# Kernel tuning notes

Measured on AMD Instinct MI355X. Metric: run time of the kernel, lower is better.

The kernel has to match this reference:

```python
import jax, jax.numpy as jnp
import numpy as np

BN_EPS = 1e-5

def _conv(x, W, b, stride, pad):
    # x: [B,C,H,W], W: [O,I,kh,kw]
    y = jax.lax.conv_general_dilated(
        x, W, window_strides=(stride, stride),
        padding=[(pad, pad), (pad, pad)],
        dimension_numbers=('NCHW', 'OIHW', 'NCHW'))
    return y + b[None, :, None, None]

def _bn(x, gamma, beta, mean, var):
    inv = gamma * jax.lax.rsqrt(var + BN_EPS)
    return x * inv[None, :, None, None] + (beta - mean * inv)[None, :, None, None]

def _haar_cD(x):
    # pywt.dwt2(x, 'haar') diagonal detail over last two axes (even H,W):
    # cD[i,j] = (x[2i,2j] - x[2i,2j+1] - x[2i+1,2j] + x[2i+1,2j+1]) / 2
    a = x[..., 0::2, 0::2]
    b = x[..., 0::2, 1::2]
    c = x[..., 1::2, 0::2]
    d = x[..., 1::2, 1::2]
    return (a - b - c + d) * 0.5

def setup_inputs() -> dict:
    key = jax.random.key(0)
    ks = jax.random.split(key, 20)
    B = 8192
    f32 = jnp.float32
    inp = {
        'x':   jax.random.normal(ks[0], (B, 3, 32, 32), dtype=f32),
        # conv1: 3 -> 32, k5 s2 p2
        'w1':  jax.random.normal(ks[1], (32, 3, 5, 5), dtype=f32) * 0.05,
        'b1':  jnp.zeros((32,), f32),
        'g1':  jnp.ones((32,), f32),
        'be1': jnp.zeros((32,), f32),
        'm1':  jax.random.normal(ks[2], (32,), dtype=f32) * 0.1,
        'v1':  jax.random.uniform(ks[3], (32,), dtype=f32, minval=0.5, maxval=1.5),
        # conv2: 32 -> 64, k3 s2 p1
        'w2':  jax.random.normal(ks[4], (64, 32, 3, 3), dtype=f32) * 0.05,
        'b2':  jnp.zeros((64,), f32),
        'g2':  jnp.ones((64,), f32),
        'be2': jnp.zeros((64,), f32),
        'm2':  jax.random.normal(ks[5], (64,), dtype=f32) * 0.1,
        'v2':  jax.random.uniform(ks[6], (64,), dtype=f32, minval=0.5, maxval=1.5),
        # attention conv: 64 -> 1, k1
        'wa':  jax.random.normal(ks[7], (1, 64, 1, 1), dtype=f32) * 0.1,
        'ba':  jnp.zeros((1,), f32),
        # decoder linears (torch Linear layout: [out, in])
        'wd1': jax.random.normal(ks[8], (512, 64 * 8 * 8), dtype=f32) * 0.02,
        'bd1': jnp.zeros((512,), f32),
        'wd2': jax.random.normal(ks[9], (128, 512), dtype=f32) * 0.04,
        'bd2': jnp.zeros((128,), f32),
    }
    return inp

def reference(x, w1, b1, g1, be1, m1, v1, w2, b2, g2, be2, m2, v2,
              wa, ba, wd1, bd1, wd2, bd2):
    # wavelet_conv stem
    h = jax.nn.relu(_bn(_conv(x, w1, b1, 2, 2), g1, be1, m1, v1))   # [B,32,16,16]
    feat = jax.nn.relu(_bn(_conv(h, w2, b2, 2, 1), g2, be2, m2, v2))  # [B,64,8,8]
    # Haar DWT diagonal-detail gate (detached in the original)
    cD = jax.lax.stop_gradient(_haar_cD(feat))                        # [B,64,4,4]
    cD_up = jnp.repeat(jnp.repeat(cD, 2, axis=-2), 2, axis=-1)        # [B,64,8,8]
    feat = feat * cD_up
    # attention gate
    attn = jax.nn.sigmoid(_conv(feat, wa, ba, 1, 0))                  # [B,1,8,8]
    feat = feat * attn
    # decode
    f = feat.reshape(feat.shape[0], -1)                               # [B,4096]
    h1 = jax.nn.relu(f @ wd1.T + bd1)                                  # [B,512]
    return jax.nn.sigmoid(h1 @ wd2.T + bd2)                            # [B,128]
```

## Files before the change

### kernel.cpp

```cpp
#include <hip/hip_runtime.h>
#include <hip/hip_bf16.h>

typedef __bf16 bf16x8 __attribute__((ext_vector_type(8)));
typedef __bf16 bf16x4 __attribute__((ext_vector_type(4)));
typedef float f32x4 __attribute__((ext_vector_type(4)));

#define BN_EPS 1e-5f

__device__ __forceinline__ void gl_lds16(const __bf16* g, __bf16* l) {
    __builtin_amdgcn_global_load_lds(
        (const __attribute__((address_space(1))) unsigned int*)g,
        (__attribute__((address_space(3))) unsigned int*)l,
        16, 0, 0);
}

__global__ __launch_bounds__(256) void wd1p_kernel(const float* __restrict__ wd1, __bf16* __restrict__ o) {
    __shared__ float t2[64][65];
    const int n = blockIdx.x;
    const int tid = threadIdx.x;
    const float* src = wd1 + (size_t)n * 4096;
    #pragma unroll
    for (int r = 0; r < 16; ++r) {
        int j = r * 256 + tid;
        t2[j & 63][j >> 6] = src[j];
    }
    __syncthreads();
    __bf16* dst = o + (size_t)n * 4096;
    #pragma unroll
    for (int r = 0; r < 16; ++r) {
        int t = r * 256 + tid;
        dst[t] = (__bf16)t2[t >> 6][t & 63];
    }
}

__global__ void prep_kernel(const float* __restrict__ wd2, const float* __restrict__ w1,
                            const float* __restrict__ w2,
                            __bf16* __restrict__ wd2o, __bf16* __restrict__ w1o,
                            __bf16* __restrict__ w2o) {
    int i = blockIdx.x * 256 + threadIdx.x;
    if (i < 65536) { wd2o[i] = (__bf16)wd2[i]; return; }
    i -= 65536;
    if (i < 4096) {
        int oc = i >> 7, rem = i & 127;
        int ot = rem >> 3, j = rem & 7;
        float v = 0.f;
        if (ot < 15 && j < 5) {
            int ic = ot / 5, ky = ot % 5;
            v = w1[((oc * 3 + ic) * 5 + ky) * 5 + j];
        }
        w1o[i] = (__bf16)v;
        return;
    }
    i -= 4096;
    if (i < 18432) {
        int oc = i / 288, rem = i % 288;
        int tap = rem / 32, ic = rem % 32;
        w2o[i] = (__bf16)w2[(oc * 32 + ic) * 9 + tap];
    }
}

__global__ __launch_bounds__(512, 2) void conv_fused_kernel(
    const float* __restrict__ x,
    const __bf16* __restrict__ w1r, const float* __restrict__ b1,
    const float* __restrict__ g1, const float* __restrict__ be1,
    const float* __restrict__ m1, const float* __restrict__ v1,
    const __bf16* __restrict__ w2r, const float* __restrict__ b2,
    const float* __restrict__ g2, const float* __restrict__ be2,
    const float* __restrict__ m2, const float* __restrict__ v2,
    const float* __restrict__ wa, const float* __restrict__ ba,
    __bf16* __restrict__ f)
{
    __shared__ __align__(16) __bf16 xsb2[2][3 * 36 * 40];
    __shared__ __align__(16) char  ubuf2[2][23552];

    const int tid  = threadIdx.x;
    const int half = tid >> 8;
    const int t    = tid & 255;
    __bf16* xsb  = xsb2[half];
    char*   ubuf = ubuf2[half];
    __bf16* hsf  = (__bf16*)ubuf;
    float*  feat = (float*)ubuf;
    float*  cds  = (float*)(ubuf + 17408);
    float*  atn  = (float*)(ubuf + 22528);

    const int b    = blockIdx.x * 2 + half;
    const int lane = t & 63;
    const int wave = t >> 6;
    const int lo   = lane >> 4;
    const int ln   = lane & 15;

    {
        bf16x8 z = {};
        for (int i = t; i < 540; i += 256) *(bf16x8*)&xsb[i * 8] = z;
        if (t < 132) {
            int pi = t >> 2, ch = t & 3;
            int pix = (pi < 17) ? pi : (pi - 16) * 17;
            *(bf16x8*)&hsf[pix * 40 + ch * 8] = z;
        }
    }
    __syncthreads();

    {
        const float4* xb = (const float4*)(x + (size_t)b * 3072);
        #pragma unroll
        for (int r = 0; r < 3; ++r) {
            int c = r * 256 + t;
            int plane = c >> 8, rem = c & 255;
            int row = rem >> 3, c4 = rem & 7;
            float4 v = xb[c];
            bf16x4 h;
            h[0] = (__bf16)v.x; h[1] = (__bf16)v.y; h[2] = (__bf16)v.z; h[3] = (__bf16)v.w;
            *(bf16x4*)&xsb[plane * 1440 + (row + 2) * 40 + 4 + c4 * 4] = h;
        }
    }

    bf16x8 bw1[2][4];
    #pragma unroll
    for (int nt = 0; nt < 2; ++nt)
        #pragma unroll
        for (int s = 0; s < 4; ++s)
            bw1[nt][s] = *(const bf16x8*)(w1r + (nt * 16 + ln) * 128 + (s * 4 + lo) * 8);
    __syncthreads();

    f32x4 c1[4][2] = {};
    const unsigned int* xw = (const unsigned int*)xsb;
    #pragma unroll
    for (int s = 0; s < 4; ++s) {
        const int o  = s * 4 + lo;
        const int ic = (o * 205) >> 10;
        const int ky = o - ic * 5;
        const bool dummy = (o == 15);
        const int icc = dummy ? 2 : ic;
        #pragma unroll
        for (int mt = 0; mt < 4; ++mt) {
            const int oy  = wave * 4 + mt;
            const int row = dummy ? 35 : (2 * oy + ky);
            const int dw  = icc * 720 + row * 20 + ln + 1;
            union { unsigned int u[4]; bf16x8 v; } fa;
            fa.u[0] = xw[dw]; fa.u[1] = xw[dw + 1]; fa.u[2] = xw[dw + 2]; fa.u[3] = 0;
            #pragma unroll
            for (int nt = 0; nt < 2; ++nt)
                c1[mt][nt] = __builtin_amdgcn_mfma_f32_16x16x32_bf16(fa.v, bw1[nt][s], c1[mt][nt], 0, 0, 0);
        }
    }

    #pragma unroll
    for (int nt = 0; nt < 2; ++nt) {
        const int oc  = nt * 16 + ln;
        const float inv = g1[oc] * rsqrtf(v1[oc] + BN_EPS);
        const float bb  = be1[oc] + (b1[oc] - m1[oc]) * inv;
        #pragma unroll
        for (int mt = 0; mt < 4; ++mt) {
            const int hy = wave * 4 + mt + 1;
            #pragma unroll
            for (int r = 0; r < 4; ++r) {
                const int hx = lo * 4 + r + 1;
                hsf[(hy * 17 + hx) * 40 + oc] = (__bf16)fmaxf(c1[mt][nt][r] * inv + bb, 0.f);
            }
        }
    }

    const int wm = wave >> 1, wn = wave & 1;
    bf16x8 bw2[2][9];
    #pragma unroll
    for (int nt = 0; nt < 2; ++nt) {
        const __bf16* wp = w2r + (wn * 32 + nt * 16 + ln) * 288 + lo * 8;
        #pragma unroll
        for (int ks = 0; ks < 9; ++ks)
            bw2[nt][ks] = *(const bf16x8*)(wp + ks * 32);
    }
    __syncthreads();

    f32x4 c2[2][2] = {};
    {
        int pixbase[2];
        #pragma unroll
        for (int mt = 0; mt < 2; ++mt) {
            int p = wm * 32 + mt * 16 + ln;
            int qy = p >> 3, qx = p & 7;
            pixbase[mt] = (2 * qy * 17 + 2 * qx) * 40 + lo * 8;
        }
        #pragma unroll
        for (int ks = 0; ks < 9; ++ks) {
            const int ty = ks / 3, tx = ks % 3;
            bf16x8 af[2];
            #pragma unroll
            for (int mt = 0; mt < 2; ++mt)
                af[mt] = *(const bf16x8*)&hsf[pixbase[mt] + (ty * 17 + tx) * 40];
            #pragma unroll
            for (int mt = 0; mt < 2; ++mt)
                #pragma unroll
                for (int nt = 0; nt < 2; ++nt)
                    c2[mt][nt] = __builtin_amdgcn_mfma_f32_16x16x32_bf16(af[mt], bw2[nt][ks], c2[mt][nt], 0, 0, 0);
        }
    }
    __syncthreads();

    #pragma unroll
    for (int nt = 0; nt < 2; ++nt) {
        const int oc  = wn * 32 + nt * 16 + ln;
        const float inv = g2[oc] * rsqrtf(v2[oc] + BN_EPS);
        const float bb  = be2[oc] + (b2[oc] - m2[oc]) * inv;
        #pragma unroll
        for (int mt = 0; mt < 2; ++mt) {
            const int p0 = wm * 32 + mt * 16 + lo * 4;
            f32x4 o;
            #pragma unroll
            for (int r = 0; r < 4; ++r)
                o[r] = fmaxf(c2[mt][nt][r] * inv + bb, 0.f);
            *(f32x4*)&feat[oc * 68 + p0] = o;
        }
    }
    __syncthreads();

    {
        const int c = t >> 2, y = t & 3;
        const float* fr = feat + c * 68 + 16 * y;
        f32x4 t0 = *(const f32x4*)(fr);
        f32x4 t2v = *(const f32x4*)(fr + 4);
        f32x4 t1 = *(const f32x4*)(fr + 8);
        f32x4 t3 = *(const f32x4*)(fr + 12);
        f32x4 o;
        o[0] = 0.5f * (t0[0] - t0[1] - t1[0] + t1[1]);
        o[1] = 0.5f * (t0[2] - t0[3] - t1[2] + t1[3]);
        o[2] = 0.5f * (t2v[0] - t2v[1] - t3[0] + t3[1]);
        o[3] = 0.5f * (t2v[2] - t2v[3] - t3[2] + t3[3]);
        *(f32x4*)&cds[c * 20 + y * 4] = o;
    }
    __syncthreads();

    const int q  = t & 63;
    const int g  = wave;
    const int qy2 = q >> 3, qx2 = q & 7;
    const int qq = (qy2 >> 1) * 4 + (qx2 >> 1);
    float a2[16];
    float part = 0.f;
    #pragma unroll
    for (int j = 0; j < 16; ++j) {
        int oc = g * 16 + j;
        float v = feat[oc * 68 + q] * cds[oc * 20 + qq];
        a2[j] = v;
        part += v * wa[oc];
    }
    atn[g * 64 + q] = part;
    __syncthreads();
    float s2  = atn[q] + atn[64 + q] + atn[128 + q] + atn[192 + q] + ba[0];
    float sig = 1.f / (1.f + __expf(-s2));

    bf16x8 fo0, fo1;
    #pragma unroll
    for (int j = 0; j < 8; ++j) {
        fo0[j] = (__bf16)(a2[j] * sig);
        fo1[j] = (__bf16)(a2[j + 8] * sig);
    }
    __bf16* fb = f + (size_t)b * 4096 + q * 64 + g * 16;
    *(bf16x8*)fb = fo0;
    *(bf16x8*)(fb + 8) = fo1;
}

__global__ __launch_bounds__(256, 4) void gemm1_split_kernel(
    const __bf16* __restrict__ A, const __bf16* __restrict__ B,
    float* __restrict__ P)
{
    const int K = 4096, NOUT = 512, KH = 2048;
    __shared__ __align__(16) __bf16 As[64][64];
    __shared__ __align__(16) __bf16 Bs[128][64];
    const int tid  = threadIdx.x;
    const int lane = tid & 63;
    const int wave = tid >> 6;
    const int lo = lane >> 4, ln = lane & 15;
    const int bid = blockIdx.x;
    const int swz = (bid & 7) * 128 + (bid >> 3);
    const int n0  = (swz & 3) * 128;
    const int zz  = (swz >> 2) & 1;
    const int m0  = (swz >> 3) * 64;
    const int ks0 = zz * KH;
    const int sw = ln & 7;
    f32x4 acc[4][2] = {};
    for (int k0 = ks0; k0 < ks0 + KH; k0 += 64) {
        #pragma unroll
        for (int r = 0; r < 2; ++r) {
            int i = r * 256 + tid;
            int row = i >> 3, cs = i & 7;
            gl_lds16(A + (size_t)(m0 + row) * K + k0 + (cs ^ (row & 7)) * 8, &As[0][0] + i * 8);
        }
        #pragma unroll
        for (int r = 0; r < 4; ++r) {
            int i = r * 256 + tid;
            int row = i >> 3, cs = i & 7;
            gl_lds16(B + (size_t)(n0 + row) * K + k0 + (cs ^ (row & 7)) * 8, &Bs[0][0] + i * 8);
        }
        __syncthreads();
        #pragma unroll
        for (int s = 0; s < 2; ++s) {
            const int c = s * 4 + lo;
            const int slot = (c ^ sw) * 8;
            bf16x8 af[4], bfr[2];
            #pragma unroll
            for (int mt = 0; mt < 4; ++mt)
                af[mt] = *(const bf16x8*)(&As[mt * 16 + ln][slot]);
            #pragma unroll
            for (int nt = 0; nt < 2; ++nt)
                bfr[nt] = *(const bf16x8*)(&Bs[wave * 32 + nt * 16 + ln][slot]);
            #pragma unroll
            for (int mt = 0; mt < 4; ++mt)
                #pragma unroll
                for (int nt = 0; nt < 2; ++nt)
                    acc[mt][nt] = __builtin_amdgcn_mfma_f32_16x16x32_bf16(af[mt], bfr[nt], acc[mt][nt], 0, 0, 0);
        }
        __syncthreads();
    }
    float* Pp = P + (size_t)zz * 8192 * 512;
    #pragma unroll
    for (int mt = 0; mt < 4; ++mt)
        #pragma unroll
        for (int nt = 0; nt < 2; ++nt)
            #pragma unroll
            for (int r = 0; r < 4; ++r) {
                int m = m0 + mt * 16 + lo * 4 + r;
                int n = n0 + wave * 32 + nt * 16 + ln;
                Pp[(size_t)m * NOUT + n] = acc[mt][nt][r];
            }
}

__global__ __launch_bounds__(256) void gemm1_kernel(
    const __bf16* __restrict__ A, const __bf16* __restrict__ B,
    const float* __restrict__ bias, __bf16* __restrict__ C)
{
    const int K = 4096, NOUT = 512;
    __shared__ __align__(16) __bf16 As[64][64];
    __shared__ __align__(16) __bf16 Bs[128][64];
    const int tid  = threadIdx.x;
    const int lane = tid & 63;
    const int wave = tid >> 6;
    const int lo = lane >> 4, ln = lane & 15;
    const int bid = blockIdx.x;
    const int swz = (bid & 7) * 64 + (bid >> 3);
    const int n0  = (swz & 3) * 128;
    const int m0  = (swz >> 2) * 64;
    const int sw = ln & 7;
    f32x4 acc[4][2] = {};
    for (int k0 = 0; k0 < K; k0 += 64) {
        #pragma unroll
        for (int r = 0; r < 2; ++r) {
            int i = r * 256 + tid;
            int row = i >> 3, cs = i & 7;
            gl_lds16(A + (size_t)(m0 + row) * K + k0 + (cs ^ (row & 7)) * 8, &As[0][0] + i * 8);
        }
        #pragma unroll
        for (int r = 0; r < 4; ++r) {
            int i = r * 256 + tid;
            int row = i >> 3, cs = i & 7;
            gl_lds16(B + (size_t)(n0 + row) * K + k0 + (cs ^ (row & 7)) * 8, &Bs[0][0] + i * 8);
        }
        __syncthreads();
        #pragma unroll
        for (int s = 0; s < 2; ++s) {
            const int c = s * 4 + lo;
            const int slot = (c ^ sw) * 8;
            bf16x8 af[4], bfr[2];
            #pragma unroll
            for (int mt = 0; mt < 4; ++mt)
                af[mt] = *(const bf16x8*)(&As[mt * 16 + ln][slot]);
            #pragma unroll
            for (int nt = 0; nt < 2; ++nt)
                bfr[nt] = *(const bf16x8*)(&Bs[wave * 32 + nt * 16 + ln][slot]);
            #pragma unroll
            for (int mt = 0; mt < 4; ++mt)
                #pragma unroll
                for (int nt = 0; nt < 2; ++nt)
                    acc[mt][nt] = __builtin_amdgcn_mfma_f32_16x16x32_bf16(af[mt], bfr[nt], acc[mt][nt], 0, 0, 0);
        }
        __syncthreads();
    }
    #pragma unroll
    for (int mt = 0; mt < 4; ++mt)
        #pragma unroll
        for (int nt = 0; nt < 2; ++nt)
            #pragma unroll
            for (int r = 0; r < 4; ++r) {
                int m = m0 + mt * 16 + lo * 4 + r;
                int n = n0 + wave * 32 + nt * 16 + ln;
                float v = acc[mt][nt][r] + bias[n];
                C[(size_t)m * NOUT + n] = (__bf16)fmaxf(v, 0.f);
            }
}

__global__ __launch_bounds__(256, 4) void gemm2_kernel(
    const __bf16* __restrict__ A, const float* __restrict__ P,
    const float* __restrict__ bd1, const __bf16* __restrict__ B,
    const float* __restrict__ bias, float* __restrict__ Out, int fused)
{
    const int K = 512, NOUT = 128;
    __shared__ __align__(16) __bf16 As[32][64];
    __shared__ __align__(16) __bf16 Bs[128][64];
    const int tid  = threadIdx.x;
    const int lane = tid & 63;
    const int wave = tid >> 6;
    const int lo = lane >> 4, ln = lane & 15;
    const int m0 = blockIdx.x * 32;
    const int sw = ln & 7;
    const size_t HALF = (size_t)8192 * 512;
    f32x4 acc[2][2] = {};
    for (int k0 = 0; k0 < K; k0 += 64) {
        {
            int i = tid;
            int row = i >> 3, cs = i & 7;
            int k = k0 + (cs ^ (row & 7)) * 8;
            if (fused) {
                const float* p0 = P + (size_t)(m0 + row) * K + k;
                f32x4 a0 = *(const f32x4*)(p0);
                f32x4 a1 = *(const f32x4*)(p0 + 4);
                f32x4 c0 = *(const f32x4*)(p0 + HALF);
                f32x4 c1 = *(const f32x4*)(p0 + HALF + 4);
                f32x4 b0 = *(const f32x4*)(bd1 + k);
                f32x4 b1v = *(const f32x4*)(bd1 + k + 4);
                bf16x8 o;
                #pragma unroll
                for (int j = 0; j < 4; ++j) {
                    o[j]     = (__bf16)fmaxf(a0[j] + c0[j] + b0[j], 0.f);
                    o[j + 4] = (__bf16)fmaxf(a1[j] + c1[j] + b1v[j], 0.f);
                }
                *(bf16x8*)(&As[0][0] + i * 8) = o;
            } else {
                gl_lds16(A + (size_t)(m0 + row) * K + k, &As[0][0] + i * 8);
            }
        }
        #pragma unroll
        for (int r = 0; r < 4; ++r) {
            int i = r * 256 + tid;
            int row = i >> 3, cs = i & 7;
            gl_lds16(B + (size_t)row * K + k0 + (cs ^ (row & 7)) * 8, &Bs[0][0] + i * 8);
        }
        __syncthreads();
        #pragma unroll
        for (int s = 0; s < 2; ++s) {
            const int c = s * 4 + lo;
            const int slot = (c ^ sw) * 8;
            bf16x8 af[2], bfr[2];
            #pragma unroll
            for (int mt = 0; mt < 2; ++mt)
                af[mt] = *(const bf16x8*)(&As[mt * 16 + ln][slot]);
            #pragma unroll
            for (int nt = 0; nt < 2; ++nt)
                bfr[nt] = *(const bf16x8*)(&Bs[wave * 32 + nt * 16 + ln][slot]);
            #pragma unroll
            for (int mt = 0; mt < 2; ++mt)
                #pragma unroll
                for (int nt = 0; nt < 2; ++nt)
                    acc[mt][nt] = __builtin_amdgcn_mfma_f32_16x16x32_bf16(af[mt], bfr[nt], acc[mt][nt], 0, 0, 0);
        }
        __syncthreads();
    }
    #pragma unroll
    for (int mt = 0; mt < 2; ++mt)
        #pragma unroll
        for (int nt = 0; nt < 2; ++nt)
            #pragma unroll
            for (int r = 0; r < 4; ++r) {
                int m = m0 + mt * 16 + lo * 4 + r;
                int n = wave * 32 + nt * 16 + ln;
                float v = acc[mt][nt][r] + bias[n];
                Out[(size_t)m * NOUT + n] = 1.f / (1.f + __expf(-v));
            }
}

extern "C" void kernel_launch(void* const* d_in, const int* in_sizes, int n_in,
                              void* d_out, int out_size, void* d_ws, size_t ws_size,
                              hipStream_t stream)
{
    const float* x   = (const float*)d_in[0];
    const float* w1  = (const float*)d_in[1];
    const float* b1  = (const float*)d_in[2];
    const float* g1  = (const float*)d_in[3];
    const float* be1 = (const float*)d_in[4];
    const float* m1  = (const float*)d_in[5];
    const float* v1  = (const float*)d_in[6];
    const float* w2  = (const float*)d_in[7];
    const float* b2  = (const float*)d_in[8];
    const float* g2  = (const float*)d_in[9];
    const float* be2 = (const float*)d_in[10];
    const float* m2  = (const float*)d_in[11];
    const float* v2  = (const float*)d_in[12];
    const float* wa  = (const float*)d_in[13];
    const float* ba  = (const float*)d_in[14];
    const float* wd1 = (const float*)d_in[15];
    const float* bd1 = (const float*)d_in[16];
    const float* wd2 = (const float*)d_in[17];
    const float* bd2 = (const float*)d_in[18];

    char* ws = (char*)d_ws;
    const size_t SZ_F  = 67108864;
    const size_t SZ_P  = 33554432;
    const size_t SZ_H1 = 8388608;
    const bool use_split = ws_size >= (SZ_F + SZ_P + SZ_H1 + 4194304 + 131072 + 65536 + 8192);

    __bf16* f_bf = (__bf16*)ws;
    float*  P;
    __bf16* h1_bf;
    char* tail;
    if (use_split) {
        P      = (float*)(ws + SZ_F);
        h1_bf  = (__bf16*)(ws + SZ_F + SZ_P);
        tail   = ws + SZ_F + SZ_P + SZ_H1;
    } else {
        P      = nullptr;
        h1_bf  = (__bf16*)(ws + SZ_F);
        tail   = ws + SZ_F + SZ_H1;
    }
    __bf16* wd1_bf = (__bf16*)tail;
    __bf16* wd2_bf = (__bf16*)(tail + 4194304);
    __bf16* w2r_bf = (__bf16*)(tail + 4194304 + 131072);
    __bf16* w1r_bf = (__bf16*)(tail + 4194304 + 131072 + 65536);

    prep_kernel<<<344, 256, 0, stream>>>(wd2, w1, w2, wd2_bf, w1r_bf, w2r_bf);
    wd1p_kernel<<<512, 256, 0, stream>>>(wd1, wd1_bf);

    conv_fused_kernel<<<4096, 512, 0, stream>>>(x, w1r_bf, b1, g1, be1, m1, v1,
                                                w2r_bf, b2, g2, be2, m2, v2, wa, ba, f_bf);

    if (use_split) {
        gemm1_split_kernel<<<1024, 256, 0, stream>>>(f_bf, wd1_bf, P);
        gemm2_kernel<<<256, 256, 0, stream>>>(nullptr, P, bd1, wd2_bf, bd2, (float*)d_out, 1);
    } else {
        gemm1_kernel<<<512, 256, 0, stream>>>(f_bf, wd1_bf, bd1, h1_bf);
        gemm2_kernel<<<256, 256, 0, stream>>>(h1_bf, nullptr, bd1, wd2_bf, bd2, (float*)d_out, 0);
    }
}
```

Before: 311.2 us.

## Split conv blocks to one image each and double-buffer split GEMM1 LDS tiles

The fused conv kernel now launches one 256-thread block per image instead of packing two images into a 512-thread block, with launch bounds set for 5 blocks per CU. This gives the scheduler finer-grained blocks and makes each block independent of the other image's barriers. The split-K GEMM1 kernel double-buffers its A/B LDS tiles so the next K-slice's global-to-LDS loads are issued before the MFMAs on the current slice run. In exchange it doubles LDS per block and drops the occupancy hint from 4 to 3.

```diff
diff --git a/kernel.cpp b/kernel.cpp
--- a/kernel.cpp
+++ b/kernel.cpp
@@ -59,7 +59,7 @@
     }
 }
 
-__global__ __launch_bounds__(512, 2) void conv_fused_kernel(
+__global__ __launch_bounds__(256, 5) void conv_fused_kernel(
     const float* __restrict__ x,
     const __bf16* __restrict__ w1r, const float* __restrict__ b1,
     const float* __restrict__ g1, const float* __restrict__ be1,
@@ -70,30 +70,25 @@
     const float* __restrict__ wa, const float* __restrict__ ba,
     __bf16* __restrict__ f)
 {
-    __shared__ __align__(16) __bf16 xsb2[2][3 * 36 * 40];
-    __shared__ __align__(16) char  ubuf2[2][23552];
-
-    const int tid  = threadIdx.x;
-    const int half = tid >> 8;
-    const int t    = tid & 255;
-    __bf16* xsb  = xsb2[half];
-    char*   ubuf = ubuf2[half];
+    __shared__ __align__(16) __bf16 xsb[3 * 36 * 40];
+    __shared__ __align__(16) char  ubuf[23552];
     __bf16* hsf  = (__bf16*)ubuf;
     float*  feat = (float*)ubuf;
     float*  cds  = (float*)(ubuf + 17408);
     float*  atn  = (float*)(ubuf + 22528);
 
-    const int b    = blockIdx.x * 2 + half;
-    const int lane = t & 63;
-    const int wave = t >> 6;
+    const int b    = blockIdx.x;
+    const int tid  = threadIdx.x;
+    const int lane = tid & 63;
+    const int wave = tid >> 6;
     const int lo   = lane >> 4;
     const int ln   = lane & 15;
 
     {
         bf16x8 z = {};
-        for (int i = t; i < 540; i += 256) *(bf16x8*)&xsb[i * 8] = z;
-        if (t < 132) {
-            int pi = t >> 2, ch = t & 3;
+        for (int i = tid; i < 540; i += 256) *(bf16x8*)&xsb[i * 8] = z;
+        if (tid < 132) {
+            int pi = tid >> 2, ch = tid & 3;
             int pix = (pi < 17) ? pi : (pi - 16) * 17;
             *(bf16x8*)&hsf[pix * 40 + ch * 8] = z;
         }
@@ -104,7 +99,7 @@
         const float4* xb = (const float4*)(x + (size_t)b * 3072);
         #pragma unroll
         for (int r = 0; r < 3; ++r) {
-            int c = r * 256 + t;
+            int c = r * 256 + tid;
             int plane = c >> 8, rem = c & 255;
             int row = rem >> 3, c4 = rem & 7;
             float4 v = xb[c];
@@ -214,7 +209,7 @@
     __syncthreads();
 
     {
-        const int c = t >> 2, y = t & 3;
+        const int c = tid >> 2, y = tid & 3;
         const float* fr = feat + c * 68 + 16 * y;
         f32x4 t0 = *(const f32x4*)(fr);
         f32x4 t2v = *(const f32x4*)(fr + 4);
@@ -229,7 +224,7 @@
     }
     __syncthreads();
 
-    const int q  = t & 63;
+    const int q  = tid & 63;
     const int g  = wave;
     const int qy2 = q >> 3, qx2 = q & 7;
     const int qq = (qy2 >> 1) * 4 + (qx2 >> 1);
@@ -258,13 +253,13 @@
     *(bf16x8*)(fb + 8) = fo1;
 }
 
-__global__ __launch_bounds__(256, 4) void gemm1_split_kernel(
+__global__ __launch_bounds__(256, 3) void gemm1_split_kernel(
     const __bf16* __restrict__ A, const __bf16* __restrict__ B,
     float* __restrict__ P)
 {
     const int K = 4096, NOUT = 512, KH = 2048;
-    __shared__ __align__(16) __bf16 As[64][64];
-    __shared__ __align__(16) __bf16 Bs[128][64];
+    __shared__ __align__(16) __bf16 As[2][64][64];
+    __shared__ __align__(16) __bf16 Bs[2][128][64];
     const int tid  = threadIdx.x;
     const int lane = tid & 63;
     const int wave = tid >> 6;
@@ -276,21 +271,48 @@
     const int m0  = (swz >> 3) * 64;
     const int ks0 = zz * KH;
     const int sw = ln & 7;
+
+    const int arow = tid >> 3, acs = tid & 7;
+    const int aks  = (acs ^ (arow & 7)) * 8;
+    const int brow = tid >> 3, bcs = tid & 7;
+
     f32x4 acc[4][2] = {};
-    for (int k0 = ks0; k0 < ks0 + KH; k0 += 64) {
+
+    {
+        const int k0 = ks0;
         #pragma unroll
         for (int r = 0; r < 2; ++r) {
             int i = r * 256 + tid;
             int row = i >> 3, cs = i & 7;
-            gl_lds16(A + (size_t)(m0 + row) * K + k0 + (cs ^ (row & 7)) * 8, &As[0][0] + i * 8);
+            gl_lds16(A + (size_t)(m0 + row) * K + k0 + (cs ^ (row & 7)) * 8, &As[0][0][0] + i * 8);
         }
         #pragma unroll
         for (int r = 0; r < 4; ++r) {
             int i = r * 256 + tid;
             int row = i >> 3, cs = i & 7;
-            gl_lds16(B + (size_t)(n0 + row) * K + k0 + (cs ^ (row & 7)) * 8, &Bs[0][0] + i * 8);
-        }
-        __syncthreads();
+            gl_lds16(B + (size_t)(n0 + row) * K + k0 + (cs ^ (row & 7)) * 8, &Bs[0][0][0] + i * 8);
+        }
+    }
+    __syncthreads();
+
+    int cur = 0;
+    for (int k0 = ks0; k0 < ks0 + KH; k0 += 64) {
+        const int nxt = cur ^ 1;
+        if (k0 + 64 < ks0 + KH) {
+            const int k1 = k0 + 64;
+            #pragma unroll
+            for (int r = 0; r < 2; ++r) {
+                int i = r * 256 + tid;
+                int row = i >> 3, cs = i & 7;
+                gl_lds16(A + (size_t)(m0 + row) * K + k1 + (cs ^ (row & 7)) * 8, &As[nxt][0][0] + i * 8);
+            }
+            #pragma unroll
+            for (int r = 0; r < 4; ++r) {
+                int i = r * 256 + tid;
+                int row = i >> 3, cs = i & 7;
+                gl_lds16(B + (size_t)(n0 + row) * K + k1 + (cs ^ (row & 7)) * 8, &Bs[nxt][0][0] + i * 8);
+            }
+        }
         #pragma unroll
         for (int s = 0; s < 2; ++s) {
             const int c = s * 4 + lo;
@@ -298,10 +320,10 @@
             bf16x8 af[4], bfr[2];
             #pragma unroll
             for (int mt = 0; mt < 4; ++mt)
-                af[mt] = *(const bf16x8*)(&As[mt * 16 + ln][slot]);
+                af[mt] = *(const bf16x8*)(&As[cur][mt * 16 + ln][slot]);
             #pragma unroll
             for (int nt = 0; nt < 2; ++nt)
-                bfr[nt] = *(const bf16x8*)(&Bs[wave * 32 + nt * 16 + ln][slot]);
+                bfr[nt] = *(const bf16x8*)(&Bs[cur][wave * 32 + nt * 16 + ln][slot]);
             #pragma unroll
             for (int mt = 0; mt < 4; ++mt)
                 #pragma unroll
@@ -309,7 +331,9 @@
                     acc[mt][nt] = __builtin_amdgcn_mfma_f32_16x16x32_bf16(af[mt], bfr[nt], acc[mt][nt], 0, 0, 0);
         }
         __syncthreads();
-    }
+        cur = nxt;
+    }
+
     float* Pp = P + (size_t)zz * 8192 * 512;
     #pragma unroll
     for (int mt = 0; mt < 4; ++mt)
@@ -516,7 +540,7 @@
     prep_kernel<<<344, 256, 0, stream>>>(wd2, w1, w2, wd2_bf, w1r_bf, w2r_bf);
     wd1p_kernel<<<512, 256, 0, stream>>>(wd1, wd1_bf);
 
-    conv_fused_kernel<<<4096, 512, 0, stream>>>(x, w1r_bf, b1, g1, be1, m1, v1,
+    conv_fused_kernel<<<8192, 256, 0, stream>>>(x, w1r_bf, b1, g1, be1, m1, v1,
                                                 w2r_bf, b2, g2, be2, m2, v2, wa, ba, f_bf);
 
     if (use_split) {
```

After: 318.0 us. 2.2% more time.

## Split conv kernel to one sample per block and merge prep launches

Applied to the files above, without the earlier changes.

Conv kernel now processes one sample per 256-thread block rather than two samples per 512-thread block, with launch bounds requesting 5 blocks per CU, so finer-grained blocks can improve occupancy and scheduling. The two weight-prep kernels are merged into a single launch that dispatches by block index to remove one launch. The stricter occupancy hint may force register spilling, and each block still carries its own LDS buffers.

```diff
diff --git a/kernel.cpp b/kernel.cpp
--- a/kernel.cpp
+++ b/kernel.cpp
@@ -14,30 +14,33 @@
         16, 0, 0);
 }
 
-__global__ __launch_bounds__(256) void wd1p_kernel(const float* __restrict__ wd1, __bf16* __restrict__ o) {
+__global__ __launch_bounds__(256) void prep_all_kernel(
+    const float* __restrict__ wd1, __bf16* __restrict__ wd1o,
+    const float* __restrict__ wd2, const float* __restrict__ w1,
+    const float* __restrict__ w2,
+    __bf16* __restrict__ wd2o, __bf16* __restrict__ w1o,
+    __bf16* __restrict__ w2o)
+{
     __shared__ float t2[64][65];
-    const int n = blockIdx.x;
     const int tid = threadIdx.x;
-    const float* src = wd1 + (size_t)n * 4096;
-    #pragma unroll
-    for (int r = 0; r < 16; ++r) {
-        int j = r * 256 + tid;
-        t2[j & 63][j >> 6] = src[j];
-    }
-    __syncthreads();
-    __bf16* dst = o + (size_t)n * 4096;
-    #pragma unroll
-    for (int r = 0; r < 16; ++r) {
-        int t = r * 256 + tid;
-        dst[t] = (__bf16)t2[t >> 6][t & 63];
-    }
-}
-
-__global__ void prep_kernel(const float* __restrict__ wd2, const float* __restrict__ w1,
-                            const float* __restrict__ w2,
-                            __bf16* __restrict__ wd2o, __bf16* __restrict__ w1o,
-                            __bf16* __restrict__ w2o) {
-    int i = blockIdx.x * 256 + threadIdx.x;
+    if (blockIdx.x < 512) {
+        const int n = blockIdx.x;
+        const float* src = wd1 + (size_t)n * 4096;
+        #pragma unroll
+        for (int r = 0; r < 16; ++r) {
+            int j = r * 256 + tid;
+            t2[j & 63][j >> 6] = src[j];
+        }
+        __syncthreads();
+        __bf16* dst = wd1o + (size_t)n * 4096;
+        #pragma unroll
+        for (int r = 0; r < 16; ++r) {
+            int t = r * 256 + tid;
+            dst[t] = (__bf16)t2[t >> 6][t & 63];
+        }
+        return;
+    }
+    int i = (blockIdx.x - 512) * 256 + tid;
     if (i < 65536) { wd2o[i] = (__bf16)wd2[i]; return; }
     i -= 65536;
     if (i < 4096) {
@@ -59,7 +62,7 @@
     }
 }
 
-__global__ __launch_bounds__(512, 2) void conv_fused_kernel(
+__global__ __launch_bounds__(256, 5) void conv_fused_kernel(
     const float* __restrict__ x,
     const __bf16* __restrict__ w1r, const float* __restrict__ b1,
     const float* __restrict__ g1, const float* __restrict__ be1,
@@ -70,30 +73,25 @@
     const float* __restrict__ wa, const float* __restrict__ ba,
     __bf16* __restrict__ f)
 {
-    __shared__ __align__(16) __bf16 xsb2[2][3 * 36 * 40];
-    __shared__ __align__(16) char  ubuf2[2][23552];
-
-    const int tid  = threadIdx.x;
-    const int half = tid >> 8;
-    const int t    = tid & 255;
-    __bf16* xsb  = xsb2[half];
-    char*   ubuf = ubuf2[half];
+    __shared__ __align__(16) __bf16 xsb[3 * 36 * 40];
+    __shared__ __align__(16) char  ubuf[23552];
     __bf16* hsf  = (__bf16*)ubuf;
     float*  feat = (float*)ubuf;
     float*  cds  = (float*)(ubuf + 17408);
     float*  atn  = (float*)(ubuf + 22528);
 
-    const int b    = blockIdx.x * 2 + half;
-    const int lane = t & 63;
-    const int wave = t >> 6;
+    const int b    = blockIdx.x;
+    const int tid  = threadIdx.x;
+    const int lane = tid & 63;
+    const int wave = tid >> 6;
     const int lo   = lane >> 4;
     const int ln   = lane & 15;
 
     {
         bf16x8 z = {};
-        for (int i = t; i < 540; i += 256) *(bf16x8*)&xsb[i * 8] = z;
-        if (t < 132) {
-            int pi = t >> 2, ch = t & 3;
+        for (int i = tid; i < 540; i += 256) *(bf16x8*)&xsb[i * 8] = z;
+        if (tid < 132) {
+            int pi = tid >> 2, ch = tid & 3;
             int pix = (pi < 17) ? pi : (pi - 16) * 17;
             *(bf16x8*)&hsf[pix * 40 + ch * 8] = z;
         }
@@ -104,7 +102,7 @@
         const float4* xb = (const float4*)(x + (size_t)b * 3072);
         #pragma unroll
         for (int r = 0; r < 3; ++r) {
-            int c = r * 256 + t;
+            int c = r * 256 + tid;
             int plane = c >> 8, rem = c & 255;
             int row = rem >> 3, c4 = rem & 7;
             float4 v = xb[c];
@@ -214,7 +212,7 @@
     __syncthreads();
 
     {
-        const int c = t >> 2, y = t & 3;
+        const int c = tid >> 2, y = tid & 3;
         const float* fr = feat + c * 68 + 16 * y;
         f32x4 t0 = *(const f32x4*)(fr);
         f32x4 t2v = *(const f32x4*)(fr + 4);
@@ -229,7 +227,7 @@
     }
     __syncthreads();
 
-    const int q  = t & 63;
+    const int q  = tid & 63;
     const int g  = wave;
     const int qy2 = q >> 3, qx2 = q & 7;
     const int qq = (qy2 >> 1) * 4 + (qx2 >> 1);
@@ -513,10 +511,9 @@
     __bf16* w2r_bf = (__bf16*)(tail + 4194304 + 131072);
     __bf16* w1r_bf = (__bf16*)(tail + 4194304 + 131072 + 65536);
 
-    prep_kernel<<<344, 256, 0, stream>>>(wd2, w1, w2, wd2_bf, w1r_bf, w2r_bf);
-    wd1p_kernel<<<512, 256, 0, stream>>>(wd1, wd1_bf);
-
-    conv_fused_kernel<<<4096, 512, 0, stream>>>(x, w1r_bf, b1, g1, be1, m1, v1,
+    prep_all_kernel<<<856, 256, 0, stream>>>(wd1, wd1_bf, wd2, w1, w2, wd2_bf, w1r_bf, w2r_bf);
+
+    conv_fused_kernel<<<8192, 256, 0, stream>>>(x, w1r_bf, b1, g1, be1, m1, v1,
                                                 w2r_bf, b2, g2, be2, m2, v2, wa, ba, f_bf);
 
     if (use_split) {
```

Measured after the change: 303.5 us. -2.5%, faster.
